# Kernel tuning notes

Hardware: AMD Instinct MI355X
Metric: run time of the kernel (lower is better)

The kernel has to match this reference:

```python
import jax, jax.numpy as jnp
import numpy as np
import math

V = 32000      # vocab_size
D = 1024       # hidden_dims
T_MAX = 1024   # max_txt_len
L = 4          # n_layers
H = 8          # heads (fixed in CausalMHA)
HD = D // H
B, T = 2, 1024
EPS = 1e-5


def setup_inputs() -> dict:
    key = jax.random.key(0)
    ks = jax.random.split(key, 20)
    s = 0.02
    inp = {
        "x": jax.random.randint(ks[0], (B, T), 0, V, dtype=jnp.int64) if jax.config.read("jax_enable_x64") else jax.random.randint(ks[0], (B, T), 0, V, dtype=jnp.int32),
        "tok_emb": jax.random.normal(ks[1], (V, D), jnp.float32) * s,
        "pos_emb": jax.random.normal(ks[2], (1, T_MAX, D), jnp.float32) * s,
        "ln1_g": jnp.ones((L, D), jnp.float32),
        "ln1_b": jnp.zeros((L, D), jnp.float32),
        "wqkv": jax.random.normal(ks[3], (L, D, 3 * D), jnp.float32) * s,
        "bqkv": jnp.zeros((L, 3 * D), jnp.float32),
        "wo": jax.random.normal(ks[4], (L, D, D), jnp.float32) * s,
        "bo": jnp.zeros((L, D), jnp.float32),
        "ln2_g": jnp.ones((L, D), jnp.float32),
        "ln2_b": jnp.zeros((L, D), jnp.float32),
        "wfc": jax.random.normal(ks[5], (L, D, 4 * D), jnp.float32) * s,   # no bias
        "wfc2": jax.random.normal(ks[6], (L, 4 * D, D), jnp.float32) * s,  # no bias
        "fn_g": jnp.ones((D,), jnp.float32),
        "fn_b": jnp.zeros((D,), jnp.float32),
        "wout": jax.random.normal(ks[7], (D, V), jnp.float32) * s,
        "bout": jnp.zeros((V,), jnp.float32),
    }
    return inp


def _ln(x, g, b):
    mu = jnp.mean(x, axis=-1, keepdims=True)
    var = jnp.var(x, axis=-1, keepdims=True)
    return (x - mu) * jax.lax.rsqrt(var + EPS) * g + b


def _attn(xn, wqkv_l, bqkv_l, wo_l, bo_l):
    Bb, Tt, _ = xn.shape
    qkv = xn @ wqkv_l + bqkv_l                      # [B,T,3D]
    q, k, v = jnp.split(qkv, 3, axis=-1)
    q = q.reshape(Bb, Tt, H, HD)
    k = k.reshape(Bb, Tt, H, HD)
    v = v.reshape(Bb, Tt, H, HD)
    scores = jnp.einsum("bqhd,bkhd->bhqk", q, k) / math.sqrt(HD)
    mask = jnp.triu(jnp.ones((Tt, Tt), bool), k=1)   # True above diagonal
    scores = jnp.where(mask, jnp.float32(-jnp.inf), scores)
    att = jax.nn.softmax(scores, axis=-1)
    out = jnp.einsum("bhqk,bkhd->bqhd", att, v).reshape(Bb, Tt, D)
    return out @ wo_l + bo_l


def reference(x, tok_emb, pos_emb, ln1_g, ln1_b, wqkv, bqkv, wo, bo,
              ln2_g, ln2_b, wfc, wfc2, fn_g, fn_b, wout, bout):
    Tt = x.shape[1]
    h = tok_emb[x] + pos_emb[:, :Tt, :]              # [B,T,D]
    for i in range(L):
        h = h + _attn(_ln(h, ln1_g[i], ln1_b[i]), wqkv[i], bqkv[i], wo[i], bo[i])
        hn = _ln(h, ln2_g[i], ln2_b[i])
        h = h + jax.nn.gelu(hn @ wfc[i], approximate=False) @ wfc2[i]
    h = _ln(h, fn_g, fn_b)
    return h @ wout + bout                           # [B,T,V] logits
```

## Files before the change

kernel.cpp:

```cpp
#include <hip/hip_runtime.h>
#include <math.h>
#include <stdint.h>

#define D_  1024
#define T_  1024
#define H_  8
#define HD_ 128
#define L_  4
#define V_  32000
#define M_  2048

typedef __attribute__((ext_vector_type(4))) float f32x4;
typedef __attribute__((ext_vector_type(4))) short s16x4;
typedef __attribute__((ext_vector_type(8))) short s16x8;
typedef unsigned short u16;

__device__ __forceinline__ u16 f2bf(float f) {
  union { float f; uint32_t u; } c; c.f = f;
  uint32_t r = c.u + 0x7fffu + ((c.u >> 16) & 1u);
  return (u16)(r >> 16);
}
__device__ __forceinline__ float bf2f(u16 h) {
  union { uint32_t u; float f; } c; c.u = ((uint32_t)h) << 16;
  return c.f;
}
__device__ __forceinline__ float gelu_f(float x) {
  return 0.5f * x * (1.0f + erff(x * 0.70710678118654752f));
}

__device__ __forceinline__ void gload16(const u16* g, u16* l) {
  __builtin_amdgcn_global_load_lds(
      (const __attribute__((address_space(1))) void*)(uintptr_t)g,
      (__attribute__((address_space(3))) void*)(uint32_t)(uintptr_t)l,
      16, 0, 0);
}

__device__ __forceinline__ void convT_f32_tile(const float* __restrict__ in,
                                               u16* __restrict__ out,
                                               int ldin, int ldout,
                                               int c0, int r0,
                                               u16 (*tile)[72])
{
  const int t = threadIdx.x;
  const int rr = t >> 2, cs = (t & 3) << 4;
  u16 tmp[16];
  const float* p = in + (size_t)(r0 + rr) * ldin + c0 + cs;
#pragma unroll
  for (int q = 0; q < 4; ++q) {
    f32x4 v = *(const f32x4*)(p + q * 4);
#pragma unroll
    for (int j = 0; j < 4; ++j) tmp[q * 4 + j] = f2bf(v[j]);
  }
  *(s16x8*)&tile[rr][cs]     = *(const s16x8*)tmp;
  *(s16x8*)&tile[rr][cs + 8] = *(const s16x8*)(tmp + 8);
  __syncthreads();
  const int cr = t >> 2, rs = (t & 3) << 4;
  u16 o[16];
#pragma unroll
  for (int j = 0; j < 16; ++j) o[j] = tile[rs + j][cr];
  u16* op = out + (size_t)(c0 + cr) * ldout + r0 + rs;
  *(s16x8*)op       = *(const s16x8*)o;
  *(s16x8*)(op + 8) = *(const s16x8*)(o + 8);
}

__device__ __forceinline__
void ln_row_body(int row, float* __restrict__ hbuf, const float* __restrict__ P,
                 const float* __restrict__ g, const float* __restrict__ b,
                 u16* __restrict__ y, int red, float* red_s)
{
  const int tid = threadIdx.x;
  const size_t i = (size_t)row * D_ + tid * 4;
  f32x4 v = *(const f32x4*)&hbuf[i];
  if (red) {
#pragma unroll
    for (int zp = 0; zp < 4; ++zp) {
      f32x4 p = *(const f32x4*)&P[(size_t)zp * M_ * D_ + i];
      v[0] += p[0]; v[1] += p[1]; v[2] += p[2]; v[3] += p[3];
    }
    *(f32x4*)&hbuf[i] = v;
  }
  float s  = v[0] + v[1] + v[2] + v[3];
  float s2 = v[0]*v[0] + v[1]*v[1] + v[2]*v[2] + v[3]*v[3];
#pragma unroll
  for (int off = 32; off > 0; off >>= 1) {
    s  += __shfl_xor(s, off);
    s2 += __shfl_xor(s2, off);
  }
  if ((tid & 63) == 0) { red_s[tid >> 6] = s; red_s[4 + (tid >> 6)] = s2; }
  __syncthreads();
  s  = red_s[0] + red_s[1] + red_s[2] + red_s[3];
  s2 = red_s[4] + red_s[5] + red_s[6] + red_s[7];
  const float mean = s * (1.0f / D_);
  const float var  = s2 * (1.0f / D_) - mean * mean;
  const float rs   = rsqrtf(var + 1e-5f);
  f32x4 gg = *(const f32x4*)&g[tid * 4];
  f32x4 bb = *(const f32x4*)&b[tid * 4];
  u16 o[4];
#pragma unroll
  for (int j = 0; j < 4; ++j) o[j] = f2bf((v[j] - mean) * rs * gg[j] + bb[j]);
  *(s16x4*)&y[i] = *(const s16x4*)o;
}

__global__ __launch_bounds__(256)
void conv4ln_kernel(const float* __restrict__ wqkv_l, const float* __restrict__ wo_l,
                    const float* __restrict__ wfc_l, const float* __restrict__ wfc2_l,
                    u16* __restrict__ Wq, u16* __restrict__ Wo,
                    u16* __restrict__ Wf1, u16* __restrict__ Wf2,
                    float* __restrict__ hbuf, const float* __restrict__ P,
                    const float* __restrict__ g, const float* __restrict__ b,
                    u16* __restrict__ y, int red)
{
  __shared__ __align__(16) u16 tile[64][72];
  int f = blockIdx.x;
  if (f < 2048) { ln_row_body(f, hbuf, P, g, b, y, red, (float*)tile); return; }
  f -= 2048;
  if (f < 768) {
    convT_f32_tile(wqkv_l, Wq, 3 * D_, D_, (f % 48) << 6, (f / 48) << 6, tile);
  } else if (f < 1024) {
    f -= 768;
    convT_f32_tile(wo_l, Wo, D_, D_, (f & 15) << 6, (f >> 4) << 6, tile);
  } else if (f < 2048) {
    f -= 1024;
    convT_f32_tile(wfc_l, Wf1, 4 * D_, D_, (f & 63) << 6, (f >> 6) << 6, tile);
  } else {
    f -= 2048;
    convT_f32_tile(wfc2_l, Wf2, D_, 4 * D_, (f & 15) << 6, (f >> 4) << 6, tile);
  }
}

__global__ __launch_bounds__(256)
void convwout_ln(const float* __restrict__ wout, u16* __restrict__ WoutT,
                 float* __restrict__ hbuf, const float* __restrict__ P,
                 const float* __restrict__ g, const float* __restrict__ b,
                 u16* __restrict__ y)
{
  __shared__ __align__(16) u16 tile[64][72];
  int f = blockIdx.x;
  if (f < 2048) { ln_row_body(f, hbuf, P, g, b, y, 1, (float*)tile); return; }
  f -= 2048;
  convT_f32_tile(wout, WoutT, V_, D_, (f % 500) << 6, (f / 500) << 6, tile);
}

__global__ __launch_bounds__(256)
void ln_fold2(float* __restrict__ hbuf, const float* __restrict__ P,
              const float* __restrict__ bo, const float* __restrict__ g,
              const float* __restrict__ b, u16* __restrict__ y)
{
  __shared__ float red_s[8];
  const int row = blockIdx.x, tid = threadIdx.x;
  const size_t i = (size_t)row * D_ + tid * 4;
  f32x4 v  = *(const f32x4*)&hbuf[i];
  f32x4 p0 = *(const f32x4*)&P[i];
  f32x4 p1 = *(const f32x4*)&P[(size_t)M_ * D_ + i];
  f32x4 bb4 = *(const f32x4*)&bo[tid * 4];
#pragma unroll
  for (int j = 0; j < 4; ++j) v[j] += p0[j] + p1[j] + bb4[j];
  *(f32x4*)&hbuf[i] = v;
  float s  = v[0] + v[1] + v[2] + v[3];
  float s2 = v[0]*v[0] + v[1]*v[1] + v[2]*v[2] + v[3]*v[3];
#pragma unroll
  for (int off = 32; off > 0; off >>= 1) {
    s  += __shfl_xor(s, off);
    s2 += __shfl_xor(s2, off);
  }
  if ((tid & 63) == 0) { red_s[tid >> 6] = s; red_s[4 + (tid >> 6)] = s2; }
  __syncthreads();
  s  = red_s[0] + red_s[1] + red_s[2] + red_s[3];
  s2 = red_s[4] + red_s[5] + red_s[6] + red_s[7];
  const float mean = s * (1.0f / D_);
  const float var  = s2 * (1.0f / D_) - mean * mean;
  const float rs   = rsqrtf(var + 1e-5f);
  f32x4 gg = *(const f32x4*)&g[tid * 4];
  f32x4 bb = *(const f32x4*)&b[tid * 4];
  u16 o[4];
#pragma unroll
  for (int j = 0; j < 4; ++j) o[j] = f2bf((v[j] - mean) * rs * gg[j] + bb[j]);
  *(s16x4*)&y[i] = *(const s16x4*)o;
}

template<int TM, int ACT, int BIAS, int OUT, int VSPLIT>
__device__ __forceinline__
void gemm2_body(const u16* __restrict__ A, const u16* __restrict__ Bw,
                const float* __restrict__ bias, const float* __restrict__ res,
                void* __restrict__ Cv,
                int K, int lda, int ldb, int ldc, float scale,
                int bx, int by, u16* __restrict__ VtOut)
{
  constexpr int WN  = (TM == 128) ? 2 : 4;
  constexpr int WNW = 128 / WN;
  constexpr int NJ  = WNW / 16;
  constexpr int AR  = TM / 64;

  const int m0 = bx * TM, n0 = by * 128;
  const int ktiles = K >> 5;

  __shared__ __align__(16) u16 As[2][TM * 32];
  __shared__ __align__(16) u16 Bs[2][128 * 32];

  const int tid = threadIdx.x, lane = tid & 63, wave = tid >> 6;
  const int wm = wave / WN, wn = wave % WN;
  const int l15 = lane & 15, l4 = lane >> 4;
  const int srow = lane >> 2, scol = (lane & 3) << 3;

  f32x4 acc[4][NJ];
  const f32x4 z4 = {0.f, 0.f, 0.f, 0.f};
#pragma unroll
  for (int i = 0; i < 4; ++i)
#pragma unroll
    for (int j = 0; j < NJ; ++j) acc[i][j] = z4;

  auto stage = [&](int kt, int buf) {
    const int kc = (kt << 5) + scol;
#pragma unroll
    for (int r = 0; r < AR; ++r) {
      const int row = r * 64 + wave * 16;
      gload16(A + (size_t)(m0 + row + srow) * lda + kc, &As[buf][row * 32]);
    }
#pragma unroll
    for (int r = 0; r < 2; ++r) {
      const int row = r * 64 + wave * 16;
      gload16(Bw + (size_t)(n0 + row + srow) * ldb + kc, &Bs[buf][row * 32]);
    }
  };

  stage(0, 0);
  __syncthreads();

  for (int kt = 0; kt < ktiles; ++kt) {
    const int buf = kt & 1;
    if (kt + 1 < ktiles) stage(kt + 1, buf ^ 1);
    const u16* ap = &As[buf][(wm * 64 + l15) * 32 + (l4 << 3)];
    const u16* bp = &Bs[buf][(wn * WNW + l15) * 32 + (l4 << 3)];
    s16x8 af[4], bf[NJ];
#pragma unroll
    for (int i = 0; i < 4; ++i) af[i] = *(const s16x8*)(ap + i * (16 * 32));
#pragma unroll
    for (int j = 0; j < NJ; ++j) bf[j] = *(const s16x8*)(bp + j * (16 * 32));
#pragma unroll
    for (int i = 0; i < 4; ++i)
#pragma unroll
      for (int j = 0; j < NJ; ++j)
        acc[i][j] = __builtin_amdgcn_mfma_f32_16x16x32_bf16(af[i], bf[j], acc[i][j], 0, 0, 0);
    __syncthreads();
  }

  float* Cf = (float*)Cv;
  u16*   Ch = (u16*)Cv;
#pragma unroll
  for (int i = 0; i < 4; ++i) {
    const int row0 = m0 + wm * 64 + i * 16 + l4 * 4;
#pragma unroll
    for (int j = 0; j < NJ; ++j) {
      const int col = n0 + wn * WNW + j * 16 + l15;
      const float bv = BIAS ? bias[col] : 0.0f;
      float vv[4];
#pragma unroll
      for (int r = 0; r < 4; ++r) {
        float v = acc[i][j][r] * scale + bv;
        if (ACT) v = gelu_f(v);
        vv[r] = v;
      }
      if (VSPLIT && col >= 2048) {
        u16 o4[4];
#pragma unroll
        for (int r = 0; r < 4; ++r) o4[r] = f2bf(vv[r]);
        const int bb = row0 >> 10, t0 = row0 & 1023, c2 = col - 2048;
        *(s16x4*)&VtOut[((size_t)(bb << 10) + c2) * 1024 + t0] = *(const s16x4*)o4;
      } else {
#pragma unroll
        for (int r = 0; r < 4; ++r) {
          const size_t idx = (size_t)(row0 + r) * ldc + col;
          if (OUT == 0)      Ch[idx] = f2bf(vv[r]);
          else if (OUT == 1) Cf[idx] = vv[r];
          else               Cf[idx] = vv[r] + res[idx];
        }
      }
    }
  }
}

__device__ __forceinline__ int2 swz2d() {
  const int gx = gridDim.x, gy = gridDim.y;
  int flat = blockIdx.y * gx + blockIdx.x;
  const int nwg = gx * gy;
  int swz = (flat & 7) * (nwg >> 3) + (flat >> 3);
  return make_int2(swz % gx, swz / gx);
}

__global__ __launch_bounds__(256)
void gemm_qkv(const u16* A, const u16* Bw, const float* bias, void* Cv, u16* Vt) {
  int2 b = swz2d();
  gemm2_body<64, 0, 1, 0, 1>(A, Bw, bias, nullptr, Cv, D_, D_, D_, 3 * D_, 1.0f,
                             b.x, b.y, Vt);
}
__global__ __launch_bounds__(256)
void gemm_wo_s(const u16* __restrict__ A, const u16* __restrict__ Bw,
               float* __restrict__ P) {
  const int gx = gridDim.x, gy = gridDim.y;
  int flat = (blockIdx.z * gy + blockIdx.y) * gx + blockIdx.x;
  const int nwg = gx * gy * gridDim.z;
  int swz = (flat & 7) * (nwg >> 3) + (flat >> 3);
  const int bx = swz % gx; swz /= gx;
  const int by = swz % gy;
  const int z  = swz / gy;
  gemm2_body<64, 0, 0, 1, 0>(A + z * 512, Bw + z * 512, nullptr, nullptr,
                             P + (size_t)z * M_ * D_,
                             512, D_, D_, D_, 1.0f, bx, by, nullptr);
}

template<int OUT, int ACT>
__device__ __forceinline__
void gemm8n_body(const u16* __restrict__ A, int lda,
                 const u16* __restrict__ Bw, int ldb,
                 void* __restrict__ Cv, int ldc, int bx, int by)
{
  const int m0 = bx << 8, n0 = by << 7;

  __shared__ __align__(16) u16 lds[49152];

  const int tid = threadIdx.x, lane = tid & 63, wave = tid >> 6;
  const int wm = wave >> 1, wn = wave & 1;
  const int l15 = lane & 15, l4 = lane >> 4;

  f32x4 acc[4][4];
  const f32x4 z4 = {0.f, 0.f, 0.f, 0.f};
#pragma unroll
  for (int i = 0; i < 4; ++i)
#pragma unroll
    for (int j = 0; j < 4; ++j) acc[i][j] = z4;

  auto stgA = [&](int buf, int kt, int kh) {
    kt = (kt < 15) ? kt : 15;
    const int slot = buf * 24576 + kh * 8192;
#pragma unroll
    for (int r = 0; r < 2; ++r) {
      const int u = r * 512 + (wave << 6) + lane;
      const int rw = u >> 2, ks = u & 3;
      const int ksw = ks ^ ((rw >> 1) & 3);
      gload16(A + (size_t)(m0 + rw) * lda + (kt << 6) + (kh << 5) + (ksw << 3),
              &lds[slot + r * 4096 + (wave << 9)]);
    }
  };
  auto stgB = [&](int buf, int kt, int kh) {
    kt = (kt < 15) ? kt : 15;
    const int slot = buf * 24576 + 16384 + kh * 4096;
    const int u = (wave << 6) + lane;
    const int rw = u >> 2, ks = u & 3;
    const int ksw = ks ^ ((rw >> 1) & 3);
    gload16(Bw + (size_t)(n0 + rw) * ldb + (kt << 6) + (kh << 5) + (ksw << 3),
            &lds[slot + (wave << 9)]);
  };

  s16x8 af[4], bfr[4];

#define LDABN(bb, kk)                                                         \
  {                                                                           \
    _Pragma("unroll") for (int f = 0; f < 4; ++f) {                           \
      const int rw = wm * 64 + f * 16 + l15;                                  \
      af[f] = *(const s16x8*)&lds[(bb) + (kk) * 8192 + rw * 32 +              \
                                  ((l4 ^ ((rw >> 1) & 3)) << 3)];             \
    }                                                                         \
    _Pragma("unroll") for (int f = 0; f < 4; ++f) {                           \
      const int rn = wn * 64 + f * 16 + l15;                                  \
      bfr[f] = *(const s16x8*)&lds[(bb) + 16384 + (kk) * 4096 + rn * 32 +     \
                                   ((l4 ^ ((rn >> 1) & 3)) << 3)];            \
    }                                                                         \
  }
#define MFMAN()                                                               \
  {                                                                           \
    __builtin_amdgcn_s_barrier();                                             \
    asm volatile("s_waitcnt lgkmcnt(0)" ::: "memory");                        \
    __builtin_amdgcn_sched_barrier(0);                                        \
    __builtin_amdgcn_s_setprio(1);                                            \
    _Pragma("unroll") for (int f = 0; f < 4; ++f)                             \
      _Pragma("unroll") for (int nf = 0; nf < 4; ++nf)                        \
        acc[f][nf] = __builtin_amdgcn_mfma_f32_16x16x32_bf16(                 \
            af[f], bfr[nf], acc[f][nf], 0, 0, 0);                             \
    __builtin_amdgcn_s_setprio(0);                                            \
  }
#define BARN() __builtin_amdgcn_s_barrier()
#define VM6()  asm volatile("s_waitcnt vmcnt(6)" ::: "memory")

  stgA(0, 0, 0); stgB(0, 0, 0);
  stgA(0, 0, 1); stgB(0, 0, 1);
  stgA(1, 1, 0); stgB(1, 1, 0);
  VM6();
  BARN();

  for (int i = 0; i < 8; ++i) {
    const int t = 2 * i;
    LDABN(0, 0);
    stgA(1, t + 1, 1); stgB(1, t + 1, 1);
    MFMAN(); VM6(); BARN();
    LDABN(0, 1);
    stgA(0, t + 2, 0); stgB(0, t + 2, 0);
    MFMAN(); VM6(); BARN();
    LDABN(24576, 0);
    stgA(0, t + 2, 1); stgB(0, t + 2, 1);
    MFMAN(); VM6(); BARN();
    LDABN(24576, 1);
    stgA(1, t + 3, 0); stgB(1, t + 3, 0);
    MFMAN(); VM6(); BARN();
  }
#undef LDABN
#undef MFMAN
#undef BARN
#undef VM6

  float* Cf = (float*)Cv;
  u16*   Ch = (u16*)Cv;
#pragma unroll
  for (int mf = 0; mf < 4; ++mf) {
    const int row0 = m0 + wm * 64 + mf * 16 + l4 * 4;
#pragma unroll
    for (int nf = 0; nf < 4; ++nf) {
      const int col = n0 + wn * 64 + nf * 16 + l15;
#pragma unroll
      for (int r = 0; r < 4; ++r) {
        float v = acc[mf][nf][r];
        if (ACT) v = gelu_f(v);
        const size_t idx = (size_t)(row0 + r) * ldc + col;
        if (OUT == 0) Ch[idx] = f2bf(v);
        else          Cf[idx] = v;
      }
    }
  }
}

__global__ __launch_bounds__(512, 1)
void gemm8n_fc1(const u16* A, const u16* Bw, void* Cv) {
  int flat = blockIdx.x;
  int swz = (flat & 7) * 32 + (flat >> 3);
  gemm8n_body<0, 1>(A, 1024, Bw, 1024, Cv, 4096, swz & 7, swz >> 3);
}
__global__ __launch_bounds__(512, 1)
void gemm8n_fc2(const u16* A, const u16* Bw, float* P) {
  int flat = blockIdx.x;
  int swz = (flat & 7) * 32 + (flat >> 3);
  const int bx = swz & 7, by = (swz >> 3) & 7, z = swz >> 6;
  gemm8n_body<1, 0>(A + z * 1024, 4096, Bw + z * 1024, 4096,
                    P + (size_t)z * M_ * D_, 1024, bx, by);
}

__global__ __launch_bounds__(512, 2)
void gemm8_logits(const u16* __restrict__ A, const u16* __restrict__ Bw,
                  const float* __restrict__ bias, float* __restrict__ C)
{
  int flat = blockIdx.x;
  int swz = (flat & 7) * 125 + (flat >> 3);
  const int bx = swz & 7;
  const int by = swz >> 3;
  const int m0 = bx << 8, n0 = by << 8;

  __shared__ __align__(16) u16 lds[65536];

  const int tid = threadIdx.x, lane = tid & 63, wave = tid >> 6;
  const int wm = wave >> 2, wn = wave & 3;
  const int l15 = lane & 15, l4 = lane >> 4;

  f32x4 acc[8][4];
  const f32x4 z4 = {0.f, 0.f, 0.f, 0.f};
#pragma unroll
  for (int i = 0; i < 8; ++i)
#pragma unroll
    for (int j = 0; j < 4; ++j) acc[i][j] = z4;

  auto stg = [&](const u16* G, int rowbase, int slot, int kt, int kh) {
    kt = (kt < 15) ? kt : 15;
#pragma unroll
    for (int r = 0; r < 2; ++r) {
      const int u = r * 512 + (wave << 6) + lane;
      const int rw = u >> 2, ks = u & 3;
      const int ksw = ks ^ ((rw >> 1) & 3);
      const u16* src = G + (size_t)(rowbase + rw) * 1024 + (kt << 6) + (kh << 5) + (ksw << 3);
      gload16(src, &lds[slot + r * 4096 + (wave << 9)]);
    }
  };

  s16x8 af[4], bfr[4];

#define LDA4(bb, kk, mh)                                                      \
  {                                                                           \
    _Pragma("unroll") for (int f = 0; f < 4; ++f) {                           \
      const int rw = wm * 128 + (mh) * 64 + f * 16 + l15;                     \
      af[f] = *(const s16x8*)&lds[(bb) + (kk) * 8192 + rw * 32 +              \
                                  ((l4 ^ ((rw >> 1) & 3)) << 3)];             \
    }                                                                         \
  }
#define LDB4(bb, kk)                                                          \
  {                                                                           \
    _Pragma("unroll") for (int f = 0; f < 4; ++f) {                           \
      const int rn = wn * 64 + f * 16 + l15;                                  \
      bfr[f] = *(const s16x8*)&lds[(bb) + 16384 + (kk) * 8192 + rn * 32 +     \
                                   ((l4 ^ ((rn >> 1) & 3)) << 3)];            \
    }                                                                         \
  }
#define MFMA16(mh)                                                            \
  {                                                                           \
    __builtin_amdgcn_s_barrier();                                             \
    asm volatile("s_waitcnt lgkmcnt(0)" ::: "memory");                        \
    __builtin_amdgcn_sched_barrier(0);                                        \
    __builtin_amdgcn_s_setprio(1);                                            \
    _Pragma("unroll") for (int f = 0; f < 4; ++f)                             \
      _Pragma("unroll") for (int nf = 0; nf < 4; ++nf)                        \
        acc[(mh) * 4 + f][nf] = __builtin_amdgcn_mfma_f32_16x16x32_bf16(      \
            af[f], bfr[nf], acc[(mh) * 4 + f][nf], 0, 0, 0);                  \
    __builtin_amdgcn_s_setprio(0);                                            \
  }
#define BAR() __builtin_amdgcn_s_barrier()
#define VM4() asm volatile("s_waitcnt vmcnt(4)" ::: "memory")

  stg(A,  m0, 0,             0, 0);
  stg(Bw, n0, 16384,         0, 0);
  stg(A,  m0, 8192,          0, 1);
  stg(Bw, n0, 16384 + 8192,  0, 1);
  stg(A,  m0, 32768,         1, 0);
  stg(Bw, n0, 32768 + 16384, 1, 0);
  VM4();
  BAR();

  for (int i = 0; i < 8; ++i) {
    const int t = 2 * i;
    LDA4(0, 0, 0); LDB4(0, 0);
    stg(A, m0, 32768 + 8192, t + 1, 1);
    MFMA16(0); BAR();
    LDA4(0, 0, 1);
    stg(Bw, n0, 32768 + 24576, t + 1, 1);
    MFMA16(1); BAR();
    LDA4(0, 1, 0); LDB4(0, 1);
    stg(A, m0, 0, t + 2, 0);
    MFMA16(0); BAR();
    LDA4(0, 1, 1);
    stg(Bw, n0, 16384, t + 2, 0);
    MFMA16(1); VM4(); BAR();
    LDA4(32768, 0, 0); LDB4(32768, 0);
    stg(A, m0, 8192, t + 2, 1);
    MFMA16(0); BAR();
    LDA4(32768, 0, 1);
    stg(Bw, n0, 16384 + 8192, t + 2, 1);
    MFMA16(1); BAR();
    LDA4(32768, 1, 0); LDB4(32768, 1);
    stg(A, m0, 32768, t + 3, 0);
    MFMA16(0); BAR();
    LDA4(32768, 1, 1);
    stg(Bw, n0, 32768 + 16384, t + 3, 0);
    MFMA16(1); VM4(); BAR();
  }
#undef LDA4
#undef LDB4
#undef MFMA16
#undef BAR
#undef VM4

  float bv[4];
#pragma unroll
  for (int nf = 0; nf < 4; ++nf) bv[nf] = bias[n0 + wn * 64 + nf * 16 + l15];
#pragma unroll
  for (int mf = 0; mf < 8; ++mf) {
    const int row0 = m0 + wm * 128 + mf * 16 + l4 * 4;
#pragma unroll
    for (int nf = 0; nf < 4; ++nf) {
      const int col = n0 + wn * 64 + nf * 16 + l15;
#pragma unroll
      for (int r = 0; r < 4; ++r)
        C[(size_t)(row0 + r) * V_ + col] = acc[mf][nf][r] + bv[nf];
    }
  }
}

__global__ __launch_bounds__(128)
void flash_attn(const u16* __restrict__ qkv, const u16* __restrict__ Vt,
                u16* __restrict__ xo)
{
  int flat = blockIdx.x;
  int swz = (flat & 7) * 64 + (flat >> 3);
  const int qb = 31 - (swz & 31);
  const int z  = swz >> 5;
  const int b  = z >> 3, hh = z & 7;

  __shared__ __align__(16) u16 Ks[64 * 128];
  __shared__ __align__(16) u16 Vs[128 * 64];
  __shared__ __align__(16) u16 Ps[32 * 80];

  const int tid = threadIdx.x, lane = tid & 63, w = tid >> 6;
  const int l15 = lane & 15, l4 = lane >> 4;
  const float iscale = 0.08838834764831845f;

  const int qrow = qb * 32 + w * 16 + l15;
  const u16* qptr = qkv + ((size_t)(b * T_) + qrow) * (3 * D_) + hh * HD_;

  s16x8 bQ[4];
#pragma unroll
  for (int ks = 0; ks < 4; ++ks)
    bQ[ks] = *(const s16x8*)(qptr + ks * 32 + l4 * 8);

  f32x4 O[8];
#pragma unroll
  for (int i = 0; i < 8; ++i) O[i] = {0.f, 0.f, 0.f, 0.f};
  float m_run = -1e30f, l_run = 0.f;

  const int ntiles = (qb >> 1) + 1;
  for (int kt = 0; kt < ntiles; ++kt) {
    __syncthreads();
    {
      const int r = tid >> 1, c0 = (tid & 1) << 6;
      const u16* src = qkv + ((size_t)(b * T_) + kt * 64 + r) * (3 * D_) + D_ + hh * HD_ + c0;
#pragma unroll
      for (int u = 0; u < 8; ++u) {
        s16x8 v = *(const s16x8*)(src + u * 8);
        const int dblk = (c0 >> 3) + u;
        *(s16x8*)&Ks[r * 128 + ((dblk ^ (r & 7)) << 3)] = v;
      }
      const int d = tid;
      const u16* vsrc = Vt + ((size_t)z * HD_ + d) * T_ + kt * 64;
#pragma unroll
      for (int u = 0; u < 8; ++u) {
        s16x8 v = *(const s16x8*)(vsrc + u * 8);
        *(s16x8*)&Vs[d * 64 + ((u ^ (d & 7)) << 3)] = v;
      }
    }
    __syncthreads();

    f32x4 st[4];
#pragma unroll
    for (int mf = 0; mf < 4; ++mf) st[mf] = {0.f, 0.f, 0.f, 0.f};
#pragma unroll
    for (int ks = 0; ks < 4; ++ks) {
      s16x8 aK[4];
#pragma unroll
      for (int mf = 0; mf < 4; ++mf) {
        const int r = mf * 16 + l15;
        aK[mf] = *(const s16x8*)&Ks[r * 128 + ((((ks << 2) + l4) ^ (r & 7)) << 3)];
      }
#pragma unroll
      for (int mf = 0; mf < 4; ++mf)
        st[mf] = __builtin_amdgcn_mfma_f32_16x16x32_bf16(aK[mf], bQ[ks], st[mf], 0, 0, 0);
    }

    const bool diag = (kt == ntiles - 1);
    float sv[16];
    float mx = -1e30f;
#pragma unroll
    for (int mf = 0; mf < 4; ++mf)
#pragma unroll
      for (int r = 0; r < 4; ++r) {
        float s = st[mf][r] * iscale;
        if (diag) {
          const int k = kt * 64 + mf * 16 + l4 * 4 + r;
          if (k > qrow) s = -1e30f;
        }
        sv[mf * 4 + r] = s;
        mx = fmaxf(mx, s);
      }
    mx = fmaxf(mx, __shfl_xor(mx, 16));
    mx = fmaxf(mx, __shfl_xor(mx, 32));
    const float m_new = fmaxf(m_run, mx);
    const float sc_old = __expf(m_run - m_new);
    float psum = 0.f;
    u16 pb[16];
#pragma unroll
    for (int j = 0; j < 16; ++j) {
      const float p = __expf(sv[j] - m_new);
      psum += p;
      pb[j] = f2bf(p);
    }
    psum += __shfl_xor(psum, 16);
    psum += __shfl_xor(psum, 32);
    l_run = l_run * sc_old + psum;
    m_run = m_new;

    float scr[4];
#pragma unroll
    for (int r = 0; r < 4; ++r) scr[r] = __shfl(sc_old, l4 * 4 + r);
#pragma unroll
    for (int df = 0; df < 8; ++df)
#pragma unroll
      for (int r = 0; r < 4; ++r) O[df][r] *= scr[r];

    {
      const int row = w * 16 + l15;
#pragma unroll
      for (int j = 0; j < 16; ++j) {
        const int k = (j >> 2) * 16 + l4 * 4 + (j & 3);
        Ps[row * 80 + (((k >> 3) ^ (l15 & 7)) << 3) + (k & 7)] = pb[j];
      }
    }

#pragma unroll
    for (int kc = 0; kc < 2; ++kc) {
      const int prow = w * 16 + l15;
      s16x8 aP = *(const s16x8*)&Ps[prow * 80 + ((((kc << 2) + l4) ^ (l15 & 7)) << 3)];
#pragma unroll
      for (int df = 0; df < 8; ++df) {
        const int d = df * 16 + l15;
        s16x8 bV = *(const s16x8*)&Vs[d * 64 + ((((kc << 2) + l4) ^ (d & 7)) << 3)];
        O[df] = __builtin_amdgcn_mfma_f32_16x16x32_bf16(aP, bV, O[df], 0, 0, 0);
      }
    }
  }

  const float inv_l = 1.0f / l_run;
  float invr[4];
#pragma unroll
  for (int r = 0; r < 4; ++r) invr[r] = __shfl(inv_l, l4 * 4 + r);
#pragma unroll
  for (int df = 0; df < 8; ++df)
#pragma unroll
    for (int r = 0; r < 4; ++r) {
      const int row = qb * 32 + w * 16 + l4 * 4 + r;
      xo[((size_t)(b * T_) + row) * D_ + hh * HD_ + df * 16 + l15] =
          f2bf(O[df][r] * invr[r]);
    }
}

__global__ __launch_bounds__(256)
void embed_kernel(const int* __restrict__ x, const float* __restrict__ tok,
                  const float* __restrict__ pos, float* __restrict__ h)
{
  const int row = blockIdx.x, tid = threadIdx.x;
  const int t = row & (T_ - 1);
  const int id = x[row];
  f32x4 a = *(const f32x4*)&tok[(size_t)id * D_ + tid * 4];
  f32x4 p = *(const f32x4*)&pos[(size_t)t * D_ + tid * 4];
  f32x4 o = {a[0] + p[0], a[1] + p[1], a[2] + p[2], a[3] + p[3]};
  *(f32x4*)&h[(size_t)row * D_ + tid * 4] = o;
}

extern "C" void kernel_launch(void* const* d_in, const int* in_sizes, int n_in,
                              void* d_out, int out_size, void* d_ws, size_t ws_size,
                              hipStream_t stream)
{
  (void)in_sizes; (void)n_in; (void)out_size; (void)ws_size;
  const int*   x     = (const int*)  d_in[0];
  const float* tok   = (const float*)d_in[1];
  const float* pos   = (const float*)d_in[2];
  const float* ln1_g = (const float*)d_in[3];
  const float* ln1_b = (const float*)d_in[4];
  const float* wqkv  = (const float*)d_in[5];
  const float* bqkv  = (const float*)d_in[6];
  const float* wo    = (const float*)d_in[7];
  const float* bo    = (const float*)d_in[8];
  const float* ln2_g = (const float*)d_in[9];
  const float* ln2_b = (const float*)d_in[10];
  const float* wfc   = (const float*)d_in[11];
  const float* wfc2  = (const float*)d_in[12];
  const float* fn_g  = (const float*)d_in[13];
  const float* fn_b  = (const float*)d_in[14];
  const float* wout  = (const float*)d_in[15];
  const float* bout  = (const float*)d_in[16];
  float* out = (float*)d_out;

  float* h  = (float*)d_ws;
  u16* xn   = (u16*)(h + (size_t)M_ * D_);
  u16* Wq   = xn  + (size_t)M_ * D_;
  u16* Wo   = Wq  + (size_t)3 * D_ * D_;
  u16* Wf1  = Wo  + (size_t)D_ * D_;
  u16* Wf2  = Wf1 + (size_t)4 * D_ * D_;
  u16* qkv  = Wf2 + (size_t)4 * D_ * D_;
  u16* Vt   = qkv + (size_t)M_ * 3 * D_;
  u16* S    = Vt  + (size_t)2 * T_ * D_;
  float* P  = (float*)(S + (size_t)M_ * 4 * D_);
  u16* WoutT = Wq;

  embed_kernel<<<M_, 256, 0, stream>>>(x, tok, pos, h);

  for (int l = 0; l < L_; ++l) {
    conv4ln_kernel<<<5120, 256, 0, stream>>>(
        wqkv + (size_t)l * D_ * 3 * D_, wo + (size_t)l * D_ * D_,
        wfc + (size_t)l * D_ * 4 * D_, wfc2 + (size_t)l * 4 * D_ * D_,
        Wq, Wo, Wf1, Wf2,
        h, P, ln1_g + l * D_, ln1_b + l * D_, xn, l > 0 ? 1 : 0);
    gemm_qkv<<<dim3(32, 24), 256, 0, stream>>>(xn, Wq, bqkv + l * 3 * D_, qkv, Vt);
    flash_attn<<<512, 128, 0, stream>>>(qkv, Vt, xn);
    gemm_wo_s<<<dim3(32, 8, 2), 256, 0, stream>>>(xn, Wo, P);
    ln_fold2<<<M_, 256, 0, stream>>>(h, P, bo + l * D_,
                                     ln2_g + l * D_, ln2_b + l * D_, xn);
    gemm8n_fc1<<<256, 512, 0, stream>>>(xn, Wf1, S);
    gemm8n_fc2<<<256, 512, 0, stream>>>(S, Wf2, P);
  }

  convwout_ln<<<10048, 256, 0, stream>>>(wout, WoutT, h, P, fn_g, fn_b, xn);
  gemm8_logits<<<1000, 512, 0, stream>>>(xn, WoutT, bout, out);
}
```

Measured before the change: 841.6 us.

## Route QKV and output-projection GEMMs through large-tile gemm8n kernel with split-K

Removes the generic 64x128 gemm2 kernel and runs the QKV projection (with bias and the transposed V write) and the Wo projection through the templated 256x128 gemm8n pipeline. The k-tile count is now a template parameter. Wo moves to four-way split-K, so the residual/LayerNorm fold kernel now sums four partial buffers. Non-temporal stores are added for fp32 partials and logits to reduce cache pollution. The risks are lower occupancy for the small-K Wo GEMM and extra partial-buffer traffic.

```diff
diff --git a/kernel.cpp b/kernel.cpp
--- a/kernel.cpp
+++ b/kernel.cpp
@@ -26,6 +26,9 @@
 }
 __device__ __forceinline__ float gelu_f(float x) {
   return 0.5f * x * (1.0f + erff(x * 0.70710678118654752f));
+}
+__device__ __forceinline__ void nt_store(float* p, float v) {
+  __builtin_nontemporal_store(v, p);
 }
 
 __device__ __forceinline__ void gload16(const u16* g, u16* l) {
@@ -142,19 +145,22 @@
 }
 
 __global__ __launch_bounds__(256)
-void ln_fold2(float* __restrict__ hbuf, const float* __restrict__ P,
+void ln_fold4(float* __restrict__ hbuf, const float* __restrict__ P,
               const float* __restrict__ bo, const float* __restrict__ g,
               const float* __restrict__ b, u16* __restrict__ y)
 {
   __shared__ float red_s[8];
   const int row = blockIdx.x, tid = threadIdx.x;
   const size_t i = (size_t)row * D_ + tid * 4;
-  f32x4 v  = *(const f32x4*)&hbuf[i];
-  f32x4 p0 = *(const f32x4*)&P[i];
-  f32x4 p1 = *(const f32x4*)&P[(size_t)M_ * D_ + i];
+  f32x4 v = *(const f32x4*)&hbuf[i];
   f32x4 bb4 = *(const f32x4*)&bo[tid * 4];
 #pragma unroll
-  for (int j = 0; j < 4; ++j) v[j] += p0[j] + p1[j] + bb4[j];
+  for (int zp = 0; zp < 4; ++zp) {
+    f32x4 p = *(const f32x4*)&P[(size_t)zp * M_ * D_ + i];
+    v[0] += p[0]; v[1] += p[1]; v[2] += p[2]; v[3] += p[3];
+  }
+#pragma unroll
+  for (int j = 0; j < 4; ++j) v[j] += bb4[j];
   *(f32x4*)&hbuf[i] = v;
   float s  = v[0] + v[1] + v[2] + v[3];
   float s2 = v[0]*v[0] + v[1]*v[1] + v[2]*v[2] + v[3]*v[3];
@@ -171,148 +177,20 @@
   const float var  = s2 * (1.0f / D_) - mean * mean;
   const float rs   = rsqrtf(var + 1e-5f);
   f32x4 gg = *(const f32x4*)&g[tid * 4];
-  f32x4 bb = *(const f32x4*)&b[tid * 4];
+  f32x4 bbn = *(const f32x4*)&b[tid * 4];
   u16 o[4];
 #pragma unroll
-  for (int j = 0; j < 4; ++j) o[j] = f2bf((v[j] - mean) * rs * gg[j] + bb[j]);
+  for (int j = 0; j < 4; ++j) o[j] = f2bf((v[j] - mean) * rs * gg[j] + bbn[j]);
   *(s16x4*)&y[i] = *(const s16x4*)o;
 }
 
-template<int TM, int ACT, int BIAS, int OUT, int VSPLIT>
-__device__ __forceinline__
-void gemm2_body(const u16* __restrict__ A, const u16* __restrict__ Bw,
-                const float* __restrict__ bias, const float* __restrict__ res,
-                void* __restrict__ Cv,
-                int K, int lda, int ldb, int ldc, float scale,
-                int bx, int by, u16* __restrict__ VtOut)
-{
-  constexpr int WN  = (TM == 128) ? 2 : 4;
-  constexpr int WNW = 128 / WN;
-  constexpr int NJ  = WNW / 16;
-  constexpr int AR  = TM / 64;
-
-  const int m0 = bx * TM, n0 = by * 128;
-  const int ktiles = K >> 5;
-
-  __shared__ __align__(16) u16 As[2][TM * 32];
-  __shared__ __align__(16) u16 Bs[2][128 * 32];
-
-  const int tid = threadIdx.x, lane = tid & 63, wave = tid >> 6;
-  const int wm = wave / WN, wn = wave % WN;
-  const int l15 = lane & 15, l4 = lane >> 4;
-  const int srow = lane >> 2, scol = (lane & 3) << 3;
-
-  f32x4 acc[4][NJ];
-  const f32x4 z4 = {0.f, 0.f, 0.f, 0.f};
-#pragma unroll
-  for (int i = 0; i < 4; ++i)
-#pragma unroll
-    for (int j = 0; j < NJ; ++j) acc[i][j] = z4;
-
-  auto stage = [&](int kt, int buf) {
-    const int kc = (kt << 5) + scol;
-#pragma unroll
-    for (int r = 0; r < AR; ++r) {
-      const int row = r * 64 + wave * 16;
-      gload16(A + (size_t)(m0 + row + srow) * lda + kc, &As[buf][row * 32]);
-    }
-#pragma unroll
-    for (int r = 0; r < 2; ++r) {
-      const int row = r * 64 + wave * 16;
-      gload16(Bw + (size_t)(n0 + row + srow) * ldb + kc, &Bs[buf][row * 32]);
-    }
-  };
-
-  stage(0, 0);
-  __syncthreads();
-
-  for (int kt = 0; kt < ktiles; ++kt) {
-    const int buf = kt & 1;
-    if (kt + 1 < ktiles) stage(kt + 1, buf ^ 1);
-    const u16* ap = &As[buf][(wm * 64 + l15) * 32 + (l4 << 3)];
-    const u16* bp = &Bs[buf][(wn * WNW + l15) * 32 + (l4 << 3)];
-    s16x8 af[4], bf[NJ];
-#pragma unroll
-    for (int i = 0; i < 4; ++i) af[i] = *(const s16x8*)(ap + i * (16 * 32));
-#pragma unroll
-    for (int j = 0; j < NJ; ++j) bf[j] = *(const s16x8*)(bp + j * (16 * 32));
-#pragma unroll
-    for (int i = 0; i < 4; ++i)
-#pragma unroll
-      for (int j = 0; j < NJ; ++j)
-        acc[i][j] = __builtin_amdgcn_mfma_f32_16x16x32_bf16(af[i], bf[j], acc[i][j], 0, 0, 0);
-    __syncthreads();
-  }
-
-  float* Cf = (float*)Cv;
-  u16*   Ch = (u16*)Cv;
-#pragma unroll
-  for (int i = 0; i < 4; ++i) {
-    const int row0 = m0 + wm * 64 + i * 16 + l4 * 4;
-#pragma unroll
-    for (int j = 0; j < NJ; ++j) {
-      const int col = n0 + wn * WNW + j * 16 + l15;
-      const float bv = BIAS ? bias[col] : 0.0f;
-      float vv[4];
-#pragma unroll
-      for (int r = 0; r < 4; ++r) {
-        float v = acc[i][j][r] * scale + bv;
-        if (ACT) v = gelu_f(v);
-        vv[r] = v;
-      }
-      if (VSPLIT && col >= 2048) {
-        u16 o4[4];
-#pragma unroll
-        for (int r = 0; r < 4; ++r) o4[r] = f2bf(vv[r]);
-        const int bb = row0 >> 10, t0 = row0 & 1023, c2 = col - 2048;
-        *(s16x4*)&VtOut[((size_t)(bb << 10) + c2) * 1024 + t0] = *(const s16x4*)o4;
-      } else {
-#pragma unroll
-        for (int r = 0; r < 4; ++r) {
-          const size_t idx = (size_t)(row0 + r) * ldc + col;
-          if (OUT == 0)      Ch[idx] = f2bf(vv[r]);
-          else if (OUT == 1) Cf[idx] = vv[r];
-          else               Cf[idx] = vv[r] + res[idx];
-        }
-      }
-    }
-  }
-}
-
-__device__ __forceinline__ int2 swz2d() {
-  const int gx = gridDim.x, gy = gridDim.y;
-  int flat = blockIdx.y * gx + blockIdx.x;
-  const int nwg = gx * gy;
-  int swz = (flat & 7) * (nwg >> 3) + (flat >> 3);
-  return make_int2(swz % gx, swz / gx);
-}
-
-__global__ __launch_bounds__(256)
-void gemm_qkv(const u16* A, const u16* Bw, const float* bias, void* Cv, u16* Vt) {
-  int2 b = swz2d();
-  gemm2_body<64, 0, 1, 0, 1>(A, Bw, bias, nullptr, Cv, D_, D_, D_, 3 * D_, 1.0f,
-                             b.x, b.y, Vt);
-}
-__global__ __launch_bounds__(256)
-void gemm_wo_s(const u16* __restrict__ A, const u16* __restrict__ Bw,
-               float* __restrict__ P) {
-  const int gx = gridDim.x, gy = gridDim.y;
-  int flat = (blockIdx.z * gy + blockIdx.y) * gx + blockIdx.x;
-  const int nwg = gx * gy * gridDim.z;
-  int swz = (flat & 7) * (nwg >> 3) + (flat >> 3);
-  const int bx = swz % gx; swz /= gx;
-  const int by = swz % gy;
-  const int z  = swz / gy;
-  gemm2_body<64, 0, 0, 1, 0>(A + z * 512, Bw + z * 512, nullptr, nullptr,
-                             P + (size_t)z * M_ * D_,
-                             512, D_, D_, D_, 1.0f, bx, by, nullptr);
-}
-
-template<int OUT, int ACT>
+template<int OUT, int ACT, int BIAS, int VSPLIT, int KT>
 __device__ __forceinline__
 void gemm8n_body(const u16* __restrict__ A, int lda,
                  const u16* __restrict__ Bw, int ldb,
-                 void* __restrict__ Cv, int ldc, int bx, int by)
+                 const float* __restrict__ bias,
+                 void* __restrict__ Cv, int ldc, int bx, int by,
+                 u16* __restrict__ VtOut)
 {
   const int m0 = bx << 8, n0 = by << 7;
 
@@ -330,7 +208,7 @@
     for (int j = 0; j < 4; ++j) acc[i][j] = z4;
 
   auto stgA = [&](int buf, int kt, int kh) {
-    kt = (kt < 15) ? kt : 15;
+    kt = (kt < KT - 1) ? kt : (KT - 1);
     const int slot = buf * 24576 + kh * 8192;
 #pragma unroll
     for (int r = 0; r < 2; ++r) {
@@ -342,7 +220,7 @@
     }
   };
   auto stgB = [&](int buf, int kt, int kh) {
-    kt = (kt < 15) ? kt : 15;
+    kt = (kt < KT - 1) ? kt : (KT - 1);
     const int slot = buf * 24576 + 16384 + kh * 4096;
     const int u = (wave << 6) + lane;
     const int rw = u >> 2, ks = u & 3;
@@ -387,7 +265,7 @@
   VM6();
   BARN();
 
-  for (int i = 0; i < 8; ++i) {
+  for (int i = 0; i < KT / 2; ++i) {
     const int t = 2 * i;
     LDABN(0, 0);
     stgA(1, t + 1, 1); stgB(1, t + 1, 1);
@@ -407,6 +285,24 @@
 #undef BARN
 #undef VM6
 
+  if (VSPLIT && n0 >= 2048) {
+#pragma unroll
+    for (int mf = 0; mf < 4; ++mf) {
+      const int row0 = m0 + wm * 64 + mf * 16 + l4 * 4;
+      const int bb = row0 >> 10, t0 = row0 & 1023;
+#pragma unroll
+      for (int nf = 0; nf < 4; ++nf) {
+        const int col = n0 + wn * 64 + nf * 16 + l15;
+        const float bv = BIAS ? bias[col] : 0.0f;
+        u16 o4[4];
+#pragma unroll
+        for (int r = 0; r < 4; ++r) o4[r] = f2bf(acc[mf][nf][r] + bv);
+        *(s16x4*)&VtOut[((size_t)(bb << 10) + (col - 2048)) * 1024 + t0] =
+            *(const s16x4*)o4;
+      }
+    }
+    return;
+  }
   float* Cf = (float*)Cv;
   u16*   Ch = (u16*)Cv;
 #pragma unroll
@@ -415,31 +311,48 @@
 #pragma unroll
     for (int nf = 0; nf < 4; ++nf) {
       const int col = n0 + wn * 64 + nf * 16 + l15;
+      const float bv = BIAS ? bias[col] : 0.0f;
 #pragma unroll
       for (int r = 0; r < 4; ++r) {
-        float v = acc[mf][nf][r];
+        float v = acc[mf][nf][r] + bv;
         if (ACT) v = gelu_f(v);
         const size_t idx = (size_t)(row0 + r) * ldc + col;
         if (OUT == 0) Ch[idx] = f2bf(v);
-        else          Cf[idx] = v;
-      }
-    }
-  }
-}
-
+        else          nt_store(&Cf[idx], v);
+      }
+    }
+  }
+}
+
+__global__ __launch_bounds__(512, 1)
+void gemm8n_qkv(const u16* A, const u16* Bw, const float* bias, u16* C, u16* Vt) {
+  int flat = blockIdx.x;
+  int swz = (flat & 7) * 24 + (flat >> 3);
+  gemm8n_body<0, 0, 1, 1, 16>(A, 1024, Bw, 1024, bias, C, 3 * D_,
+                              swz & 7, swz >> 3, Vt);
+}
+__global__ __launch_bounds__(512, 1)
+void gemm8n_wo(const u16* A, const u16* Bw, float* P) {
+  int flat = blockIdx.x;
+  int swz = (flat & 7) * 32 + (flat >> 3);
+  const int bx = swz & 7, by = (swz >> 3) & 7, z = swz >> 6;
+  gemm8n_body<1, 0, 0, 0, 4>(A + z * 256, 1024, Bw + z * 256, 1024, nullptr,
+                             P + (size_t)z * M_ * D_, 1024, bx, by, nullptr);
+}
 __global__ __launch_bounds__(512, 1)
 void gemm8n_fc1(const u16* A, const u16* Bw, void* Cv) {
   int flat = blockIdx.x;
   int swz = (flat & 7) * 32 + (flat >> 3);
-  gemm8n_body<0, 1>(A, 1024, Bw, 1024, Cv, 4096, swz & 7, swz >> 3);
+  gemm8n_body<0, 1, 0, 0, 16>(A, 1024, Bw, 1024, nullptr, Cv, 4096,
+                              swz & 7, swz >> 3, nullptr);
 }
 __global__ __launch_bounds__(512, 1)
 void gemm8n_fc2(const u16* A, const u16* Bw, float* P) {
   int flat = blockIdx.x;
   int swz = (flat & 7) * 32 + (flat >> 3);
   const int bx = swz & 7, by = (swz >> 3) & 7, z = swz >> 6;
-  gemm8n_body<1, 0>(A + z * 1024, 4096, Bw + z * 1024, 4096,
-                    P + (size_t)z * M_ * D_, 1024, bx, by);
+  gemm8n_body<1, 0, 0, 0, 16>(A + z * 1024, 4096, Bw + z * 1024, 4096, nullptr,
+                              P + (size_t)z * M_ * D_, 1024, bx, by, nullptr);
 }
 
 __global__ __launch_bounds__(512, 2)
@@ -563,7 +476,7 @@
       const int col = n0 + wn * 64 + nf * 16 + l15;
 #pragma unroll
       for (int r = 0; r < 4; ++r)
-        C[(size_t)(row0 + r) * V_ + col] = acc[mf][nf][r] + bv[nf];
+        nt_store(&C[(size_t)(row0 + r) * V_ + col], acc[mf][nf][r] + bv[nf]);
     }
   }
 }
@@ -770,10 +683,10 @@
         wfc + (size_t)l * D_ * 4 * D_, wfc2 + (size_t)l * 4 * D_ * D_,
         Wq, Wo, Wf1, Wf2,
         h, P, ln1_g + l * D_, ln1_b + l * D_, xn, l > 0 ? 1 : 0);
-    gemm_qkv<<<dim3(32, 24), 256, 0, stream>>>(xn, Wq, bqkv + l * 3 * D_, qkv, Vt);
+    gemm8n_qkv<<<192, 512, 0, stream>>>(xn, Wq, bqkv + l * 3 * D_, qkv, Vt);
     flash_attn<<<512, 128, 0, stream>>>(qkv, Vt, xn);
-    gemm_wo_s<<<dim3(32, 8, 2), 256, 0, stream>>>(xn, Wo, P);
-    ln_fold2<<<M_, 256, 0, stream>>>(h, P, bo + l * D_,
+    gemm8n_wo<<<256, 512, 0, stream>>>(xn, Wo, P);
+    ln_fold4<<<M_, 256, 0, stream>>>(h, P, bo + l * D_,
                                      ln2_g + l * D_, ln2_b + l * D_, xn);
     gemm8n_fc1<<<256, 512, 0, stream>>>(xn, Wf1, S);
     gemm8n_fc2<<<256, 512, 0, stream>>>(S, Wf2, P);
```

Result: no change. 854.2 us (+1.5%).
